# Optimization experiments

Hardware: AMD Instinct MI355X
Metric: run time of the kernel (lower is better)

The kernel has to match this reference:

```python
import jax, jax.numpy as jnp
import numpy as np

B, L, V, DIN, H = 256, 256, 2048, 128, 256   # trees, leaves/tree, vocab, in_dim, mem_dim
NODES = 2 * L - 1                            # perfect binary tree, level-by-level layout
LEVELS = int(np.log2(L)) + 1                 # 9 levels: 256,128,...,1 nodes


def setup_inputs() -> dict:
    key = jax.random.key(0)
    ks = jax.random.split(key, 32)
    w = lambda k, shape: jax.random.normal(k, shape, jnp.float32) * 0.05
    inp = {
        "input_ids": jax.random.randint(ks[0], (B, NODES), 0, V),
        "emb": w(ks[1], (V, DIN)),
        # iou projections (i,o,u concatenated -> 3H)
        "Wioux": w(ks[2], (DIN, 3 * H)), "bioux": jnp.zeros((3 * H,), jnp.float32),
        "Wiouh1": w(ks[3], (H, 3 * H)), "biouh1": jnp.zeros((3 * H,), jnp.float32),
        "Wiouh2": w(ks[4], (H, 3 * H)), "biouh2": jnp.zeros((3 * H,), jnp.float32),
        # forget gates
        "Wfx": w(ks[5], (DIN, H)), "bfx": jnp.zeros((H,), jnp.float32),
        "Wfh11": w(ks[6], (H, H)), "bfh11": jnp.zeros((H,), jnp.float32),
        "Wfh12": w(ks[7], (H, H)), "bfh12": jnp.zeros((H,), jnp.float32),
        "Wfh21": w(ks[8], (H, H)), "bfh21": jnp.zeros((H,), jnp.float32),
        "Wfh22": w(ks[9], (H, H)), "bfh22": jnp.zeros((H,), jnp.float32),
        # classifier head
        "Wl1": w(ks[10], (H, 100)), "bl1": jnp.zeros((100,), jnp.float32),
        "Wl2": w(ks[11], (100, 1)), "bl2": jnp.zeros((1,), jnp.float32),
    }
    return inp


def reference(input_ids, emb, Wioux, bioux, Wiouh1, biouh1, Wiouh2, biouh2,
              Wfx, bfx, Wfh11, bfh11, Wfh12, bfh12, Wfh21, bfh21, Wfh22, bfh22,
              Wl1, bl1, Wl2, bl2):
    emb = emb.at[0].set(0.0)                 # padding_idx=0
    xemb = emb[input_ids]                    # [B, NODES, DIN]

    def cell(x, h1, h2, c1, c2):
        iou = (x @ Wioux + bioux) + (h1 @ Wiouh1 + biouh1) + (h2 @ Wiouh2 + biouh2)
        i, o, u = jnp.split(iou, 3, axis=-1)
        i, o, u = jax.nn.sigmoid(i), jax.nn.sigmoid(o), jnp.tanh(u)
        fx = x @ Wfx + bfx
        f0 = jax.nn.sigmoid((h1 @ Wfh11 + bfh11) + (h2 @ Wfh12 + bfh12) + fx)
        f1 = jax.nn.sigmoid((h1 @ Wfh21 + bfh21) + (h2 @ Wfh22 + bfh22) + fx)
        c = i * u + f0 * c1 + f1 * c2
        h = o * jnp.tanh(c)
        return h, c

    # leaves: zero child states
    z = jnp.zeros((B, L, H), jnp.float32)
    h, c = cell(xemb[:, :L], z, z, z, z)     # [B, L, H]

    off, n = 0, L
    for _ in range(LEVELS - 1):              # fixed small structural loop (8 iters)
        off += n
        n //= 2
        x = xemb[:, off:off + n]             # [B, n, DIN]
        h, c = cell(x, h[:, 0::2], h[:, 1::2], c[:, 0::2], c[:, 1::2])

    root_h = h[:, 0]                         # [B, H]
    hid = root_h @ Wl1 + bl1                 # linear1
    pred = (jax.nn.relu(hid) @ Wl2 + bl2)[..., 0]   # [B], arithmetic head (no softmax)
    return pred
```

## Files before the change

kernel.cpp:

```cpp
#include <hip/hip_runtime.h>
#include <math.h>

#define B_ 256
#define L_ 256
#define V_ 2048
#define DIN_ 128
#define H_ 256
#define NODES_ 511

typedef _Float16 half8 __attribute__((ext_vector_type(8)));
typedef float f32x4 __attribute__((ext_vector_type(4)));

__device__ __forceinline__ float sigm(float x) { return 1.f / (1.f + __expf(-x)); }
__device__ __forceinline__ float tanh_f(float x) {
    float xc = fminf(fmaxf(x, -15.f), 15.f);
    float e = __expf(2.f * xc);
    return (e - 1.f) / (e + 1.f);
}
__device__ __forceinline__ void gload16(const void* g, void* l) {
    __builtin_amdgcn_global_load_lds((const __attribute__((address_space(1))) unsigned int*)g,
                                     (__attribute__((address_space(3))) unsigned int*)l, 16, 0, 0);
}

__global__ void build_WTh(_Float16* __restrict__ WTh,
    const float* __restrict__ Wiouh1, const float* __restrict__ Wfh11, const float* __restrict__ Wfh21,
    const float* __restrict__ Wiouh2, const float* __restrict__ Wfh12, const float* __restrict__ Wfh22)
{
    int e = blockIdx.x * 256 + threadIdx.x;
    int nn = e >> 9, k = e & 511;
    int g = nn >> 8, t = nn & 255;
    float v;
    if (k < 256) {
        v = (g < 3) ? Wiouh1[k * 768 + nn] : ((g == 3) ? Wfh11[k * 256 + t] : Wfh21[k * 256 + t]);
    } else {
        int kp = k - 256;
        v = (g < 3) ? Wiouh2[kp * 768 + nn] : ((g == 3) ? Wfh12[kp * 256 + t] : Wfh22[kp * 256 + t]);
    }
    WTh[e] = (_Float16)v;
}

__global__ __launch_bounds__(256) void build_table(float* __restrict__ tab, const float* __restrict__ emb,
    const float* __restrict__ Wioux, const float* __restrict__ Wfx,
    const float* __restrict__ bioux, const float* __restrict__ biouh1, const float* __restrict__ biouh2,
    const float* __restrict__ bfx, const float* __restrict__ bfh11, const float* __restrict__ bfh12,
    const float* __restrict__ bfh21, const float* __restrict__ bfh22)
{
    __shared__ float As[64][33];
    __shared__ float Ws[32][65];
    const int tid = threadIdx.x, tx = tid & 15, ty = tid >> 4;
    const int i0 = blockIdx.x * 64, c0 = blockIdx.y * 64;
    const int g = c0 >> 8;
    float acc[4][4];
    #pragma unroll
    for (int i = 0; i < 4; ++i)
        #pragma unroll
        for (int j = 0; j < 4; ++j) acc[i][j] = 0.f;

    for (int k0 = 0; k0 < 128; k0 += 32) {
        #pragma unroll
        for (int it = 0; it < 2; ++it) {
            int f = tid + it * 256;
            int row = f >> 3, kk = (f & 7) * 4;
            int gr = i0 + row;
            float4 av = (gr == 0) ? make_float4(0.f, 0.f, 0.f, 0.f)
                                  : *(const float4*)(emb + (size_t)gr * 128 + k0 + kk);
            As[row][kk] = av.x; As[row][kk + 1] = av.y; As[row][kk + 2] = av.z; As[row][kk + 3] = av.w;
            int k = f >> 4, cc = (f & 15) * 4;
            int col = c0 + cc;
            float4 wv = (g < 3) ? *(const float4*)(Wioux + (size_t)(k0 + k) * 768 + col)
                                : *(const float4*)(Wfx + (size_t)(k0 + k) * 256 + (col & 255));
            Ws[k][cc] = wv.x; Ws[k][cc + 1] = wv.y; Ws[k][cc + 2] = wv.z; Ws[k][cc + 3] = wv.w;
        }
        __syncthreads();
        #pragma unroll 8
        for (int k = 0; k < 32; ++k) {
            float a[4], w[4];
            #pragma unroll
            for (int i = 0; i < 4; ++i) a[i] = As[ty * 4 + i][k];
            #pragma unroll
            for (int j = 0; j < 4; ++j) w[j] = Ws[k][tx * 4 + j];
            #pragma unroll
            for (int i = 0; i < 4; ++i)
                #pragma unroll
                for (int j = 0; j < 4; ++j) acc[i][j] = fmaf(a[i], w[j], acc[i][j]);
        }
        __syncthreads();
    }
    #pragma unroll
    for (int j = 0; j < 4; ++j) {
        int col = c0 + tx * 4 + j; int t = col & 255;
        float bs = (g < 3) ? (bioux[col] + biouh1[col] + biouh2[col])
                 : (g == 3) ? (bfx[t] + bfh11[t] + bfh12[t])
                            : (bfx[t] + bfh21[t] + bfh22[t]);
        #pragma unroll
        for (int i = 0; i < 4; ++i)
            tab[(size_t)(i0 + ty * 4 + i) * 1280 + col] = acc[i][j] + bs;
    }
}

__global__ void build_h0c0(const float* __restrict__ tab, _Float16* __restrict__ H0h, float* __restrict__ H0c) {
    int id = blockIdx.x, t = threadIdx.x;
    const float* tp = tab + (size_t)id * 1280 + t;
    float vi = sigm(tp[0]), vo = sigm(tp[256]), vu = tanh_f(tp[512]);
    float c = vi * vu;
    H0h[id * 256 + t] = (_Float16)(vo * tanh_f(c));
    H0c[id * 256 + t] = c;
}

template<bool LVL1, int RT>
__global__ __launch_bounds__(256, 3) void cellG(
    const _Float16* __restrict__ WTh, const float* __restrict__ tab,
    const int* __restrict__ ids,
    const _Float16* __restrict__ h_prev, const float* __restrict__ c_prev,
    _Float16* __restrict__ h_out, float* __restrict__ c_out,
    int n, int ln, int off, int nx)
{
    constexpr int BM = RT * 64;
    __shared__ __align__(16) char Asm[2][BM * 64];
    __shared__ __align__(16) char Bsm[2][5120];
    const int tid = threadIdx.x, lane = tid & 63, wid = tid >> 6;
    const int l15 = lane & 15, lg = lane >> 4;

    int bid = blockIdx.x, x, y;
    if ((nx & 7) == 0) { int xcd = bid & 7, rank = bid >> 3; x = xcd * (nx >> 3) + (rank >> 4); y = rank & 15; }
    else { x = bid >> 4; y = bid & 15; }
    const int rowB = x * BM;
    const int t0 = y * 16;

    const int xs = ((lane >> 2) & 3) ^ ((lane >> 4) & 3);
    const unsigned segOff = (unsigned)((((lane & 3) ^ xs)) * 16);
    unsigned srcA[RT], srcB1_[LVL1 ? RT : 1];
    #pragma unroll
    for (int i = 0; i < RT; ++i) {
        int rl = (wid * RT + i) * 16 + (lane >> 2);
        int r = rowB + rl;
        if constexpr (LVL1) {
            int b = r >> 7, j2 = r & 127;
            srcA[i]   = (unsigned)ids[b * NODES_ + 2 * j2] * 512u + segOff;
            srcB1_[i] = (unsigned)ids[b * NODES_ + 2 * j2 + 1] * 512u + segOff;
        } else {
            srcA[i] = (unsigned)r * 1024u + segOff;
        }
    }
    unsigned bsrc0, bsrc1 = 0;
    {
        int nr = tid >> 2, j = tid & 3;
        int ng = (nr >> 4) * 256 + t0 + (nr & 15);
        bsrc0 = (unsigned)((ng * 512 + ((j ^ ((nr >> 1) & 3)) * 8)) * 2);
        if (tid < 64) {
            int ng2 = 1024 + t0 + (tid >> 2);
            int seg2 = (tid & 3) ^ ((tid >> 3) & 3);
            bsrc1 = (unsigned)((ng2 * 512 + seg2 * 8) * 2);
        }
    }
    const char* hPB = (const char*)h_prev;
    const char* wPB = (const char*)WTh;

    f32x4 acc[RT][5];
    #pragma unroll
    for (int rt = 0; rt < RT; ++rt)
        #pragma unroll
        for (int g = 0; g < 5; ++g) acc[rt][g] = (f32x4)0.f;

    const int xA = (l15 & 3) ^ ((l15 >> 2) & 3);
    const int xB = (l15 >> 1) & 3;

    #pragma unroll
    for (int i = 0; i < RT; ++i)
        gload16(hPB + srcA[i], &Asm[0][(wid * RT + i) * 1024 + lane * 16]);
    gload16(wPB + bsrc0, &Bsm[0][wid * 1024 + lane * 16]);
    if (tid < 64) gload16(wPB + bsrc1, &Bsm[0][4096 + lane * 16]);
    __syncthreads();

    #pragma unroll
    for (int S = 0; S < 16; ++S) {
        const int cur = S & 1, nxt = cur ^ 1;
        if (S < 15) {
            const unsigned k1b = (unsigned)(S + 1) * 64u;
            #pragma unroll
            for (int i = 0; i < RT; ++i) {
                unsigned sa;
                if constexpr (LVL1)
                    sa = (S + 1 < 8) ? (srcA[i] + k1b) : (srcB1_[i] + k1b - 512u);
                else
                    sa = srcA[i] + k1b;
                gload16(hPB + sa, &Asm[nxt][(wid * RT + i) * 1024 + lane * 16]);
            }
            gload16(wPB + bsrc0 + k1b, &Bsm[nxt][wid * 1024 + lane * 16]);
            if (tid < 64) gload16(wPB + bsrc1 + k1b, &Bsm[nxt][4096 + lane * 16]);
        }
        half8 aF[RT];
        #pragma unroll
        for (int rt = 0; rt < RT; ++rt)
            aF[rt] = *(const half8*)&Asm[cur][(wid * RT * 16 + rt * 16 + l15) * 64 + ((lg ^ xA) * 16)];
        #pragma unroll
        for (int g = 0; g < 5; ++g) {
            half8 bF = *(const half8*)&Bsm[cur][(g * 16 + l15) * 64 + ((lg ^ xB) * 16)];
            #pragma unroll
            for (int rt = 0; rt < RT; ++rt)
                acc[rt][g] = __builtin_amdgcn_mfma_f32_16x16x32_f16(aF[rt], bF, acc[rt][g], 0, 0, 0);
        }
        __syncthreads();
    }

    const int tcol = t0 + l15;
    #pragma unroll
    for (int rt = 0; rt < RT; ++rt) {
        #pragma unroll
        for (int q = 0; q < 4; ++q) {
            int row = rowB + wid * (RT * 16) + rt * 16 + lg * 4 + q;
            int b = row >> ln, j = row & (n - 1);
            int id = ids[b * NODES_ + off + j];
            const float* tp = tab + (size_t)id * 1280 + tcol;
            float c1, c2;
            if constexpr (LVL1) {
                int bb = row >> 7, jj = row & 127;
                c1 = c_prev[(size_t)ids[bb * NODES_ + 2 * jj] * 256 + tcol];
                c2 = c_prev[(size_t)ids[bb * NODES_ + 2 * jj + 1] * 256 + tcol];
            } else {
                const float* cpp = c_prev + (size_t)row * 512 + tcol;
                c1 = cpp[0]; c2 = cpp[256];
            }
            float vi  = sigm(acc[rt][0][q] + tp[0]);
            float vo  = sigm(acc[rt][1][q] + tp[256]);
            float vu  = tanh_f(acc[rt][2][q] + tp[512]);
            float vf0 = sigm(acc[rt][3][q] + tp[768]);
            float vf1 = sigm(acc[rt][4][q] + tp[1024]);
            float c = vi * vu + vf0 * c1 + vf1 * c2;
            size_t ob = (size_t)row * 256 + tcol;
            h_out[ob] = (_Float16)(vo * tanh_f(c));
            c_out[ob] = c;
        }
    }
}

__global__ void head_kernel(const _Float16* __restrict__ hroot,
    const float* __restrict__ Wl1, const float* __restrict__ bl1,
    const float* __restrict__ Wl2, const float* __restrict__ bl2,
    float* __restrict__ out)
{
    __shared__ float hrow[H_];
    __shared__ float red[256];
    int b = blockIdx.x; int tid = threadIdx.x;
    hrow[tid] = (float)hroot[(size_t)b * H_ + tid];
    __syncthreads();
    float v = 0.f;
    if (tid < 100) {
        float s = bl1[tid];
        for (int k = 0; k < H_; ++k) s = fmaf(hrow[k], Wl1[k * 100 + tid], s);
        v = fmaxf(s, 0.f) * Wl2[tid];
    }
    red[tid] = v;
    __syncthreads();
    for (int s = 128; s > 0; s >>= 1) { if (tid < s) red[tid] += red[tid + s]; __syncthreads(); }
    if (tid == 0) out[b] = red[0] + bl2[0];
}

extern "C" void kernel_launch(void* const* d_in, const int* in_sizes, int n_in,
                              void* d_out, int out_size, void* d_ws, size_t ws_size,
                              hipStream_t stream) {
    const int*   ids    = (const int*)d_in[0];
    const float* emb    = (const float*)d_in[1];
    const float* Wioux  = (const float*)d_in[2];
    const float* bioux  = (const float*)d_in[3];
    const float* Wiouh1 = (const float*)d_in[4];
    const float* biouh1 = (const float*)d_in[5];
    const float* Wiouh2 = (const float*)d_in[6];
    const float* biouh2 = (const float*)d_in[7];
    const float* Wfx    = (const float*)d_in[8];
    const float* bfx    = (const float*)d_in[9];
    const float* Wfh11  = (const float*)d_in[10];
    const float* bfh11  = (const float*)d_in[11];
    const float* Wfh12  = (const float*)d_in[12];
    const float* bfh12  = (const float*)d_in[13];
    const float* Wfh21  = (const float*)d_in[14];
    const float* bfh21  = (const float*)d_in[15];
    const float* Wfh22  = (const float*)d_in[16];
    const float* bfh22  = (const float*)d_in[17];
    const float* Wl1    = (const float*)d_in[18];
    const float* bl1    = (const float*)d_in[19];
    const float* Wl2    = (const float*)d_in[20];
    const float* bl2    = (const float*)d_in[21];
    float* out = (float*)d_out;

    char* wsb = (char*)d_ws;
    _Float16* WTh = (_Float16*)(wsb);
    float*    tab = (float*)(wsb + 1310720);
    _Float16* H0h = (_Float16*)(wsb + 11796480);
    float*    H0c = (float*)(wsb + 12845056);
    _Float16* hA  = (_Float16*)(wsb + 14942208);
    _Float16* hB  = (_Float16*)(wsb + 23330816);
    float*    cA  = (float*)(wsb + 40108032);
    float*    cB  = (float*)(wsb + 56885248);

    build_WTh<<<dim3(2560), 256, 0, stream>>>(WTh, Wiouh1, Wfh11, Wfh21, Wiouh2, Wfh12, Wfh22);
    build_table<<<dim3(32, 20), 256, 0, stream>>>(tab, emb, Wioux, Wfx,
        bioux, biouh1, biouh2, bfx, bfh11, bfh12, bfh21, bfh22);
    build_h0c0<<<dim3(2048), 256, 0, stream>>>(tab, H0h, H0c);

    cellG<true, 4><<<dim3(2048), 256, 0, stream>>>(WTh, tab, ids, H0h, H0c, hB, cB, 128, 7, 256, 128);

    _Float16 *hp = hB, *hn = hA;
    float    *cp = cB, *cn = cA;
    int off = 384, n = 64, ln = 6;
    for (int lvl = 2; lvl <= 8; ++lvl) {
        int M = B_ * n;
        if (M >= 2048) {
            int nx = M / 256;
            cellG<false, 4><<<dim3(nx * 16), 256, 0, stream>>>(WTh, tab, ids, hp, cp, hn, cn, n, ln, off, nx);
        } else if (M >= 1024) {
            int nx = M / 128;
            cellG<false, 2><<<dim3(nx * 16), 256, 0, stream>>>(WTh, tab, ids, hp, cp, hn, cn, n, ln, off, nx);
        } else {
            int nx = M / 64;
            cellG<false, 1><<<dim3(nx * 16), 256, 0, stream>>>(WTh, tab, ids, hp, cp, hn, cn, n, ln, off, nx);
        }
        off += n; n >>= 1; --ln;
        _Float16* t1 = hp; hp = hn; hn = t1;
        float*    t2 = cp; cp = cn; cn = t2;
    }

    head_kernel<<<dim3(256), 256, 0, stream>>>(hp, Wl1, bl1, Wl2, bl2, out);
}
```

Before: 289.7 us.

## Triple-buffer cell GEMM K-loop with counted vmcnt waits instead of syncthreads

Moves the cell kernel's K-loop from double to triple buffering of the A and B LDS tiles, issuing loads two stages ahead. Per-stage __syncthreads is replaced by an explicit s_waitcnt vmcnt with a per-wave count plus s_barrier, so older async global-to-LDS loads can stay in flight. The aim is to hide global load latency better. In exchange it uses more LDS per block, and launch bounds now vary by RT (2 waves/SIMD for RT=4, 4 otherwise), which may lower occupancy for the large levels. The XOR swizzles are also unified.

```diff
diff --git a/kernel.cpp b/kernel.cpp
--- a/kernel.cpp
+++ b/kernel.cpp
@@ -20,6 +20,9 @@
 __device__ __forceinline__ void gload16(const void* g, void* l) {
     __builtin_amdgcn_global_load_lds((const __attribute__((address_space(1))) unsigned int*)g,
                                      (__attribute__((address_space(3))) unsigned int*)l, 16, 0, 0);
+}
+template<int N> __device__ __forceinline__ void vwaitN() {
+    asm volatile("s_waitcnt vmcnt(%0)" :: "i"(N) : "memory");
 }
 
 __global__ void build_WTh(_Float16* __restrict__ WTh,
@@ -108,7 +111,7 @@
 }
 
 template<bool LVL1, int RT>
-__global__ __launch_bounds__(256, 3) void cellG(
+__global__ __launch_bounds__(256, (RT >= 4 ? 2 : 4)) void cellH(
     const _Float16* __restrict__ WTh, const float* __restrict__ tab,
     const int* __restrict__ ids,
     const _Float16* __restrict__ h_prev, const float* __restrict__ c_prev,
@@ -116,8 +119,9 @@
     int n, int ln, int off, int nx)
 {
     constexpr int BM = RT * 64;
-    __shared__ __align__(16) char Asm[2][BM * 64];
-    __shared__ __align__(16) char Bsm[2][5120];
+    constexpr int AB = BM * 64;
+    __shared__ __align__(16) char Asm[3][AB];
+    __shared__ __align__(16) char Bsm[3][5120];
     const int tid = threadIdx.x, lane = tid & 63, wid = tid >> 6;
     const int l15 = lane & 15, lg = lane >> 4;
 
@@ -127,8 +131,7 @@
     const int rowB = x * BM;
     const int t0 = y * 16;
 
-    const int xs = ((lane >> 2) & 3) ^ ((lane >> 4) & 3);
-    const unsigned segOff = (unsigned)((((lane & 3) ^ xs)) * 16);
+    const unsigned segOff = (unsigned)((((lane & 3) ^ ((lane >> 3) & 3))) * 16);
     unsigned srcA[RT], srcB1_[LVL1 ? RT : 1];
     #pragma unroll
     for (int i = 0; i < RT; ++i) {
@@ -147,7 +150,7 @@
         int nr = tid >> 2, j = tid & 3;
         int ng = (nr >> 4) * 256 + t0 + (nr & 15);
         bsrc0 = (unsigned)((ng * 512 + ((j ^ ((nr >> 1) & 3)) * 8)) * 2);
-        if (tid < 64) {
+        if (wid == 0) {
             int ng2 = 1024 + t0 + (tid >> 2);
             int seg2 = (tid & 3) ^ ((tid >> 3) & 3);
             bsrc1 = (unsigned)((ng2 * 512 + seg2 * 8) * 2);
@@ -162,45 +165,50 @@
         #pragma unroll
         for (int g = 0; g < 5; ++g) acc[rt][g] = (f32x4)0.f;
 
-    const int xA = (l15 & 3) ^ ((l15 >> 2) & 3);
-    const int xB = (l15 >> 1) & 3;
-
-    #pragma unroll
-    for (int i = 0; i < RT; ++i)
-        gload16(hPB + srcA[i], &Asm[0][(wid * RT + i) * 1024 + lane * 16]);
-    gload16(wPB + bsrc0, &Bsm[0][wid * 1024 + lane * 16]);
-    if (tid < 64) gload16(wPB + bsrc1, &Bsm[0][4096 + lane * 16]);
-    __syncthreads();
-
-    #pragma unroll
-    for (int S = 0; S < 16; ++S) {
-        const int cur = S & 1, nxt = cur ^ 1;
-        if (S < 15) {
-            const unsigned k1b = (unsigned)(S + 1) * 64u;
-            #pragma unroll
-            for (int i = 0; i < RT; ++i) {
-                unsigned sa;
-                if constexpr (LVL1)
-                    sa = (S + 1 < 8) ? (srcA[i] + k1b) : (srcB1_[i] + k1b - 512u);
-                else
-                    sa = srcA[i] + k1b;
-                gload16(hPB + sa, &Asm[nxt][(wid * RT + i) * 1024 + lane * 16]);
-            }
-            gload16(wPB + bsrc0 + k1b, &Bsm[nxt][wid * 1024 + lane * 16]);
-            if (tid < 64) gload16(wPB + bsrc1 + k1b, &Bsm[nxt][4096 + lane * 16]);
-        }
+    const int xw = (l15 >> 1) & 3;
+
+    auto STAGE = [&](int st, int buf) {
+        #pragma unroll
+        for (int i = 0; i < RT; ++i) {
+            unsigned sa;
+            if constexpr (LVL1)
+                sa = (st < 8) ? (srcA[i] + (unsigned)st * 64u) : (srcB1_[i] + (unsigned)(st - 8) * 64u);
+            else
+                sa = srcA[i] + (unsigned)st * 64u;
+            gload16(hPB + sa, &Asm[buf][(wid * RT + i) * 1024 + lane * 16]);
+        }
+        gload16(wPB + bsrc0 + (unsigned)st * 64u, &Bsm[buf][tid * 16]);
+        if (wid == 0) gload16(wPB + bsrc1 + (unsigned)st * 64u, &Bsm[buf][4096 + tid * 16]);
+    };
+    auto COMPUTE = [&](int buf) {
         half8 aF[RT];
         #pragma unroll
         for (int rt = 0; rt < RT; ++rt)
-            aF[rt] = *(const half8*)&Asm[cur][(wid * RT * 16 + rt * 16 + l15) * 64 + ((lg ^ xA) * 16)];
+            aF[rt] = *(const half8*)&Asm[buf][(wid * RT * 16 + rt * 16 + l15) * 64 + ((lg ^ xw) * 16)];
         #pragma unroll
         for (int g = 0; g < 5; ++g) {
-            half8 bF = *(const half8*)&Bsm[cur][(g * 16 + l15) * 64 + ((lg ^ xB) * 16)];
+            half8 bF = *(const half8*)&Bsm[buf][(g * 16 + l15) * 64 + ((lg ^ xw) * 16)];
             #pragma unroll
             for (int rt = 0; rt < RT; ++rt)
                 acc[rt][g] = __builtin_amdgcn_mfma_f32_16x16x32_f16(aF[rt], bF, acc[rt][g], 0, 0, 0);
         }
-        __syncthreads();
+    };
+    auto WAITB = [&](bool counted) {
+        if (counted) { if (wid == 0) vwaitN<RT + 2>(); else vwaitN<RT + 1>(); }
+        else vwaitN<0>();
+        __builtin_amdgcn_s_barrier();
+        __builtin_amdgcn_sched_barrier(0);
+    };
+
+    STAGE(0, 0);
+    STAGE(1, 1);
+    WAITB(true);
+
+    #pragma unroll
+    for (int S = 0; S < 16; ++S) {
+        if (S + 2 < 16) STAGE(S + 2, (S + 2) % 3);
+        COMPUTE(S % 3);
+        if (S < 15) WAITB(S + 2 < 16);
     }
 
     const int tcol = t0 + l15;
@@ -298,7 +306,7 @@
         bioux, biouh1, biouh2, bfx, bfh11, bfh12, bfh21, bfh22);
     build_h0c0<<<dim3(2048), 256, 0, stream>>>(tab, H0h, H0c);
 
-    cellG<true, 4><<<dim3(2048), 256, 0, stream>>>(WTh, tab, ids, H0h, H0c, hB, cB, 128, 7, 256, 128);
+    cellH<true, 4><<<dim3(2048), 256, 0, stream>>>(WTh, tab, ids, H0h, H0c, hB, cB, 128, 7, 256, 128);
 
     _Float16 *hp = hB, *hn = hA;
     float    *cp = cB, *cn = cA;
@@ -307,13 +315,13 @@
         int M = B_ * n;
         if (M >= 2048) {
             int nx = M / 256;
-            cellG<false, 4><<<dim3(nx * 16), 256, 0, stream>>>(WTh, tab, ids, hp, cp, hn, cn, n, ln, off, nx);
+            cellH<false, 4><<<dim3(nx * 16), 256, 0, stream>>>(WTh, tab, ids, hp, cp, hn, cn, n, ln, off, nx);
         } else if (M >= 1024) {
             int nx = M / 128;
-            cellG<false, 2><<<dim3(nx * 16), 256, 0, stream>>>(WTh, tab, ids, hp, cp, hn, cn, n, ln, off, nx);
+            cellH<false, 2><<<dim3(nx * 16), 256, 0, stream>>>(WTh, tab, ids, hp, cp, hn, cn, n, ln, off, nx);
         } else {
             int nx = M / 64;
-            cellG<false, 1><<<dim3(nx * 16), 256, 0, stream>>>(WTh, tab, ids, hp, cp, hn, cn, n, ln, off, nx);
+            cellH<false, 1><<<dim3(nx * 16), 256, 0, stream>>>(WTh, tab, ids, hp, cp, hn, cn, n, ln, off, nx);
         }
         off += n; n >>= 1; --ln;
         _Float16* t1 = hp; hp = hn; hn = t1;
```

Result: faster. 278.0 us (-4.0%).
